# Performance work log

Measured on AMD Instinct MI355X. Metric: run time of the kernel, lower is better.

The kernel has to match this reference:

```python
import jax, jax.numpy as jnp
import numpy as np

B, T = 2, 2048
DENSE = 1024
SPARSE = 1024
NH = 8
HD = SPARSE // NH          # 128
WINDOW = 64
K = 32
RANK = HD // 4             # 32
GATE_THRESH = 0.2


def setup_inputs() -> dict:
    key = jax.random.key(0)
    ks = jax.random.split(key, 12)
    return {
        "x": jax.random.normal(ks[0], (B, T, DENSE), dtype=jnp.float32),
        "enc_q": jax.random.normal(ks[1], (NH, DENSE, HD), dtype=jnp.float32) * 0.02,
        "enc_v": jax.random.normal(ks[2], (NH, DENSE, HD), dtype=jnp.float32) * 0.02,
        # metric network: Linear(SPARSE, SPARSE//2) -> GELU -> Linear(SPARSE//2, NH*HD)
        "metric_w1": jax.random.normal(ks[3], (SPARSE, SPARSE // 2), dtype=jnp.float32) * (1.0 / np.sqrt(SPARSE)),
        "metric_b1": jnp.zeros((SPARSE // 2,), dtype=jnp.float32),
        "metric_w2": jax.random.normal(ks[4], (SPARSE // 2, NH * HD), dtype=jnp.float32) * (1.0 / np.sqrt(SPARSE // 2)),
        "metric_b2": jnp.zeros((NH * HD,), dtype=jnp.float32),
        "base_metric": jnp.ones((NH, HD), dtype=jnp.float32) * 0.1,
        "hebb_U": jax.random.normal(ks[5], (NH, HD, RANK), dtype=jnp.float32) * 0.01,
        "hebb_V": jax.random.normal(ks[6], (NH, RANK, HD), dtype=jnp.float32) * 0.01,
        "decoder": jax.random.normal(ks[7], (NH * HD, DENSE), dtype=jnp.float32) * 0.02,
    }


def _causal_window_indices(t_len, window):
    pos = jnp.arange(t_len)
    off = jnp.arange(window)
    idx = jnp.clip(pos[:, None] - off[None, :], 0, t_len - 1)  # (T, W)
    mask = idx <= pos[:, None]
    return idx, mask


def _dynamic_metric(field, w1, b1, w2, b2, base):
    # field: (B, T, SPARSE)
    sig = field.mean(axis=1)
    if field.shape[1] >= 8:
        sig = sig + field[:, ::8].mean(axis=1) * 0.5
    h = jax.nn.gelu(sig @ w1 + b1, approximate=False)
    mod = (h @ w2 + b2).reshape(field.shape[0], NH, HD)
    return jax.nn.softplus(base[None] + 0.1 * mod)  # (B, NH, HD)


def reference(x, enc_q, enc_v, metric_w1, metric_b1, metric_w2, metric_b2,
              base_metric, hebb_U, hebb_V, decoder):
    Bb, Tt, _ = x.shape
    query_sparse = jax.nn.relu(jnp.einsum('btd,nde->btne', x, enc_q))  # (B,T,NH,HD)
    value_sparse = jax.nn.relu(jnp.einsum('btd,nde->btne', x, enc_v))

    metric = _dynamic_metric(query_sparse.reshape(Bb, Tt, NH * HD),
                             metric_w1, metric_b1, metric_w2, metric_b2, base_metric)

    idx, mask = _causal_window_indices(Tt, WINDOW)  # (T,W)
    idx_b = jnp.broadcast_to(idx[None], (Bb, Tt, WINDOW))
    batch_ix = jnp.arange(Bb)[:, None, None]

    outs = []
    for h in range(NH):
        q_h = query_sparse[:, :, h, :]   # (B,T,HD)
        v_h = value_sparse[:, :, h, :]
        m_h = metric[:, h][:, None, None, :]  # (B,1,1,HD)

        k_windows = q_h[:, idx, :]            # (B,T,W,HD) gather
        diff = k_windows - q_h[:, :, None, :]
        dist = jnp.sqrt((diff * diff * m_h).sum(axis=-1) + 1e-8)  # (B,T,W)
        dist = jnp.where(mask[None], dist, jnp.inf)

        neg_d, loc = jax.lax.top_k(-dist, K)  # smallest-K distances
        topd = -neg_d
        top_idx = jnp.take_along_axis(idx_b, loc, axis=2)  # (B,T,K)

        infl = jnp.exp(-topd)
        infl = infl / (infl.sum(axis=-1, keepdims=True) + 1e-8)

        neighbor_v = v_h[batch_ix, top_idx]   # (B,T,K,HD)
        context = jnp.einsum('btk,btkd->btd', infl, neighbor_v)

        q_norm = jnp.linalg.norm(q_h, axis=-1, keepdims=True)
        gate = (q_norm > GATE_THRESH).astype(q_h.dtype)
        heb_mat = hebb_U[h] @ hebb_V[h]       # (HD,HD)
        q_unit = q_h / jnp.maximum(q_norm, 1e-12)  # F.normalize
        heb_ctx = q_unit @ heb_mat
        context = context + gate * 0.1 * heb_ctx

        outs.append(q_h * context)

    out_sparse = jnp.stack(outs, axis=2)           # (B,T,NH,HD)
    return out_sparse.reshape(Bb, Tt, NH * HD) @ decoder
```

## Files before the change

### kernel.cpp

```cpp
#include <hip/hip_runtime.h>
#include <math.h>

#define T_ 2048
#define NH_ 8
#define HD_ 128

typedef unsigned short u16;
typedef short bf16x8 __attribute__((ext_vector_type(8)));
typedef _Float16 f16x8 __attribute__((ext_vector_type(8)));
typedef float f32x4 __attribute__((ext_vector_type(4)));

union FH { _Float16 h; u16 u; };

__device__ __forceinline__ u16 f2h(float f)
{
    FH c; c.h = (_Float16)f; return c.u;
}
__device__ __forceinline__ float h2f(u16 v)
{
    FH c; c.u = v; return (float)c.h;
}
__device__ __forceinline__ void split1h(float f, u16& h, u16& l)
{
    h = f2h(f);
    l = f2h(f - h2f(h));
}

__device__ __forceinline__ u16 f2bf(float f)
{
    unsigned u = __float_as_uint(f);
    return (u16)((u + 0x7FFFu + ((u >> 16) & 1u)) >> 16);
}
__device__ __forceinline__ float bf2f(u16 h)
{
    return __uint_as_float(((unsigned)h) << 16);
}


__global__ __launch_bounds__(256) void cvt_pk(const float* __restrict__ in,
                                              u16* __restrict__ hi)
{
    int i = (blockIdx.x * 256 + threadIdx.x) * 4;
    int m = i >> 10, k = i & 1023;
    float4 v = *(const float4*)&in[i];
    ushort4 hv = {f2h(v.x), f2h(v.y), f2h(v.z), f2h(v.w)};
    long o = (long)(m >> 6) * 65536 + (k >> 5) * 2048
           + ((k >> 3) & 3) * 512 + (m & 63) * 8 + (k & 7);
    *(ushort4*)&hi[o] = hv;
}

__global__ __launch_bounds__(256) void cvt_wT_pk(const float* __restrict__ src0,
                                                 const float* __restrict__ src1,
                                                 u16* __restrict__ WTh,
                                                 int Kd, int cs, int cm, long sn, int sk)
{
    __shared__ u16 tH[32][33];
    const float* Bw = blockIdx.z ? src1 : src0;
    const int nofs = blockIdx.z << 10;
    const int tid = threadIdx.x;
    const int tx = tid & 31, ty = tid >> 5;
    const int k0 = blockIdx.x * 32, c0 = blockIdx.y * 32;
    #pragma unroll
    for (int r = 0; r < 4; ++r) {
        int k = k0 + ty * 4 + r;
        int c = c0 + tx;
        float v = Bw[(long)(c >> cs) * sn + (long)k * sk + (c & cm)];
        tH[ty * 4 + r][tx] = f2h(v);
    }
    __syncthreads();
    const long sstr = (long)Kd * 64;
    #pragma unroll
    for (int r = 0; r < 4; ++r) {
        int n = nofs + c0 + ty * 4 + r;
        int k = k0 + tx;
        long o = (long)(n >> 6) * sstr + (k >> 5) * 2048
               + ((k >> 3) & 3) * 512 + (n & 63) * 8 + (k & 7);
        WTh[o] = tH[tx][ty * 4 + r];
    }
}

__global__ __launch_bounds__(256, 1) void gemm_qv(
    const u16* __restrict__ Ah, const u16* __restrict__ Bh,
    float* __restrict__ C, float* __restrict__ Ps, float* __restrict__ Ps8,
    int N, int Kd)
{
    __shared__ __align__(16) u16 S[4][6144];

    const int tid  = threadIdx.x;
    const int w    = tid >> 6;
    const int lane = tid & 63;

    const int id   = blockIdx.x;
    const int m0   = (id & 31) * 128;
    const int n0   = (id >> 5) * 256;

    const int mw   = (w & 1) * 64, nw = (w >> 1) * 128;
    const int mr   = lane & 15, quad = lane >> 4;

    const long sstr = (long)Kd * 64;
    const u16* gAh = Ah + (long)((m0 + mw) >> 6) * sstr;
    const u16* gB0 = Bh + (long)((n0 + nw) >> 6) * sstr;
    const u16* gB1 = gB0 + sstr;

    u16* W = &S[w][0];

    f32x4 acc[4][8] = {};
    uint4 a0, a1, a2, a3;
    uint4 b0, b1, b2, b3, b4, b5, b6, b7;

#define LOADG(KT) do { long t = (long)(KT) * 2048 + lane * 8;                        \
    a0 = *(const uint4*)(gAh + t +    0); a1 = *(const uint4*)(gAh + t +  512);      \
    a2 = *(const uint4*)(gAh + t + 1024); a3 = *(const uint4*)(gAh + t + 1536);      \
    b0 = *(const uint4*)(gB0 + t +    0); b1 = *(const uint4*)(gB0 + t +  512);      \
    b2 = *(const uint4*)(gB0 + t + 1024); b3 = *(const uint4*)(gB0 + t + 1536);      \
    b4 = *(const uint4*)(gB1 + t +    0); b5 = *(const uint4*)(gB1 + t +  512);      \
    b6 = *(const uint4*)(gB1 + t + 1024); b7 = *(const uint4*)(gB1 + t + 1536); } while (0)

#define STOREG() do { u16* D = W + lane * 8;                                         \
    *(uint4*)(D +    0) = a0; *(uint4*)(D +  512) = a1;                              \
    *(uint4*)(D + 1024) = a2; *(uint4*)(D + 1536) = a3;                              \
    *(uint4*)(D + 2048) = b0; *(uint4*)(D + 2560) = b1;                              \
    *(uint4*)(D + 3072) = b2; *(uint4*)(D + 3584) = b3;                              \
    *(uint4*)(D + 4096) = b4; *(uint4*)(D + 4608) = b5;                              \
    *(uint4*)(D + 5120) = b6; *(uint4*)(D + 5632) = b7; } while (0)

    LOADG(0);
    STOREG();
    LOADG(1);

    const int NT = Kd >> 5;
    for (int kt = 0; kt < NT; ++kt) {
        f16x8 fah[4], fbh[8];
        #pragma unroll
        for (int i = 0; i < 4; ++i)
            fah[i] = *(const f16x8*)(W + quad * 512 + (i * 16 + mr) * 8);
        #pragma unroll
        for (int j = 0; j < 8; ++j)
            fbh[j] = *(const f16x8*)(W + 2048 + ((j < 4) ? 0 : 2048)
                                     + quad * 512 + ((j & 3) * 16 + mr) * 8);
        if (kt + 1 < NT) STOREG();
        if (kt + 2 < NT) LOADG(kt + 2);
        #pragma unroll
        for (int i = 0; i < 4; ++i)
            #pragma unroll
            for (int j = 0; j < 8; ++j)
                acc[i][j] = __builtin_amdgcn_mfma_f32_16x16x32_f16(fah[i], fbh[j], acc[i][j], 0, 0, 0);
    }
#undef LOADG
#undef STOREG

    #pragma unroll
    for (int i = 0; i < 4; ++i)
        #pragma unroll
        for (int j = 0; j < 8; ++j)
            #pragma unroll
            for (int r = 0; r < 4; ++r) {
                float v = fmaxf(acc[i][j][r], 0.f);
                acc[i][j][r] = v;
                int row = m0 + mw + i * 16 + quad * 4 + r;
                int col = n0 + nw + j * 16 + mr;
                C[(long)row * N + col] = v;
            }

    if (n0 < 1024) {
        int slot = (id & 31) * 2 + (w & 1);
        #pragma unroll
        for (int j = 0; j < 8; ++j) {
            float ps = 0.f, p8 = 0.f;
            #pragma unroll
            for (int i = 0; i < 4; ++i) {
                #pragma unroll
                for (int r = 0; r < 4; ++r) ps += acc[i][j][r];
                if ((quad & 1) == 0) p8 += acc[i][j][0];
            }
            ps += __shfl_xor(ps, 16, 64); ps += __shfl_xor(ps, 32, 64);
            p8 += __shfl_xor(p8, 16, 64); p8 += __shfl_xor(p8, 32, 64);
            if (quad == 0) {
                int col = n0 + nw + j * 16 + mr;
                Ps [slot * 1024 + col] = ps;
                Ps8[slot * 1024 + col] = p8;
            }
        }
    }
}

__global__ __launch_bounds__(256, 1) void gemm_dec(
    const u16* __restrict__ Ah, const u16* __restrict__ Bh,
    float* __restrict__ C, int N, int Kd)
{
    __shared__ __align__(16) u16 S[4][4096];

    const int tid  = threadIdx.x;
    const int w    = tid >> 6;
    const int lane = tid & 63;

    const int id   = blockIdx.x;
    const int m0   = (((id & 7) << 2) + ((id >> 3) & 3)) * 128;
    const int n0   = (id >> 5) * 128;

    const int mw   = (w & 1) * 64, nw = (w >> 1) * 64;
    const int mr   = lane & 15, quad = lane >> 4;

    const long sstr = (long)Kd * 64;
    const u16* gAh = Ah + (long)((m0 + mw) >> 6) * sstr;
    const u16* gBh = Bh + (long)((n0 + nw) >> 6) * sstr;

    u16* W = &S[w][0];

    f32x4 acc[4][4] = {};
    uint4 a0, a1, a2, a3, b0, b1, b2, b3;

#define LOADG(KT) do { long t = (long)(KT) * 2048 + lane * 8;                        \
    a0 = *(const uint4*)(gAh + t +    0); a1 = *(const uint4*)(gAh + t +  512);      \
    a2 = *(const uint4*)(gAh + t + 1024); a3 = *(const uint4*)(gAh + t + 1536);      \
    b0 = *(const uint4*)(gBh + t +    0); b1 = *(const uint4*)(gBh + t +  512);      \
    b2 = *(const uint4*)(gBh + t + 1024); b3 = *(const uint4*)(gBh + t + 1536); } while (0)

#define STOREG() do { u16* D = W + lane * 8;                                         \
    *(uint4*)(D +    0) = a0; *(uint4*)(D +  512) = a1;                              \
    *(uint4*)(D + 1024) = a2; *(uint4*)(D + 1536) = a3;                              \
    *(uint4*)(D + 2048) = b0; *(uint4*)(D + 2560) = b1;                              \
    *(uint4*)(D + 3072) = b2; *(uint4*)(D + 3584) = b3; } while (0)

    LOADG(0);
    STOREG();
    LOADG(1);

    const int NT = Kd >> 5;
    for (int kt = 0; kt < NT; ++kt) {
        f16x8 fah[4], fbh[4];
        #pragma unroll
        for (int i = 0; i < 4; ++i) {
            int ro = quad * 512 + (i * 16 + mr) * 8;
            fah[i] = *(const f16x8*)(W + ro);
            fbh[i] = *(const f16x8*)(W + 2048 + ro);
        }
        if (kt + 1 < NT) STOREG();
        if (kt + 2 < NT) LOADG(kt + 2);
        #pragma unroll
        for (int i = 0; i < 4; ++i)
            #pragma unroll
            for (int j = 0; j < 4; ++j)
                acc[i][j] = __builtin_amdgcn_mfma_f32_16x16x32_f16(fah[i], fbh[j], acc[i][j], 0, 0, 0);
    }
#undef LOADG
#undef STOREG

    #pragma unroll
    for (int i = 0; i < 4; ++i)
        #pragma unroll
        for (int j = 0; j < 4; ++j)
            #pragma unroll
            for (int r = 0; r < 4; ++r) {
                int row = m0 + mw + i * 16 + quad * 4 + r;
                int col = n0 + nw + j * 16 + mr;
                C[(long)row * N + col] = acc[i][j][r];
            }
}

__global__ __launch_bounds__(256) void heb_gemm(
    const u16* __restrict__ Qbf, const u16* __restrict__ MhT,
    u16* __restrict__ HEBbf)
{
    __shared__ __align__(16) u16 sA[4][128][8], sB[4][128][8];

    const int tid  = threadIdx.x;
    const int w    = tid >> 6;
    const int lane = tid & 63;
    const int m0   = blockIdx.x * 128;
    const int h    = blockIdx.y;
    const int mw   = w * 32;
    const int mr   = lane & 15, quad = lane >> 4;
    const u16* Bm  = MhT + h * 16384;

    f32x4 acc[2][8] = {};

    for (int k0 = 0; k0 < 128; k0 += 32) {
        #pragma unroll
        for (int u = 0; u < 4; ++u) {
            int c = (w & 1) * 4 + u;
            int kq = c >> 1, half = c & 1;
            const u16* src; u16* dst; long gofs;
            if (w < 2) {
                src = Qbf;
                dst = &sA[0][0][0] + kq * 1024 + half * 512;
                gofs = (long)(m0 + half * 64 + lane) * 1024 + h * 128 + k0 + kq * 8;
            } else {
                src = Bm;
                dst = &sB[0][0][0] + kq * 1024 + half * 512;
                gofs = (long)(half * 64 + lane) * 128 + k0 + kq * 8;
            }
            __builtin_amdgcn_global_load_lds(
                (const __attribute__((address_space(1))) unsigned int*)(src + gofs),
                (__attribute__((address_space(3))) unsigned int*)dst, 16, 0, 0);
        }
        __syncthreads();

        bf16x8 fa[2], fb[8];
        #pragma unroll
        for (int i = 0; i < 2; ++i)
            fa[i] = *(const bf16x8*)&sA[quad][mw + i * 16 + mr][0];
        #pragma unroll
        for (int j = 0; j < 8; ++j)
            fb[j] = *(const bf16x8*)&sB[quad][j * 16 + mr][0];
        #pragma unroll
        for (int i = 0; i < 2; ++i)
            #pragma unroll
            for (int j = 0; j < 8; ++j)
                acc[i][j] = __builtin_amdgcn_mfma_f32_16x16x32_bf16(fa[i], fb[j], acc[i][j], 0, 0, 0);
        __syncthreads();
    }

    #pragma unroll
    for (int i = 0; i < 2; ++i)
        #pragma unroll
        for (int j = 0; j < 8; ++j)
            #pragma unroll
            for (int r = 0; r < 4; ++r) {
                int row = m0 + mw + i * 16 + quad * 4 + r;
                int col = h * 128 + j * 16 + mr;
                HEBbf[(long)row * 1024 + col] = f2bf(acc[i][j][r]);
            }
}

__global__ __launch_bounds__(256) void qu_stage(const float* __restrict__ QV,
                                                const float* __restrict__ Me,
                                                u16* __restrict__ Qbf,
                                                u16* __restrict__ Uh, u16* __restrict__ Ul,
                                                float* __restrict__ nArr)
{
    int gid4 = (blockIdx.x * 256 + threadIdx.x) * 4;
    int e4 = gid4 & 127;
    int t  = (gid4 >> 7) & 2047;
    int bh = gid4 >> 18;
    int b  = bh >> 3, h = bh & 7;
    float4 q = *(const float4*)&QV[((long)(b * 2048 + t)) * 2048 + h * 128 + e4];
    ushort4 qo = {f2bf(q.x), f2bf(q.y), f2bf(q.z), f2bf(q.w)};
    *(ushort4*)&Qbf[((long)(b * 2048 + t)) * 1024 + h * 128 + e4] = qo;

    float4 m = *(const float4*)&Me[bh * 128 + e4];
    float ux = sqrtf(m.x) * q.x, uy = sqrtf(m.y) * q.y;
    float uz = sqrtf(m.z) * q.z, uw = sqrtf(m.w) * q.w;
    u16 h0, l0, h1, l1, h2, l2, h3, l3;
    split1h(ux, h0, l0); split1h(uy, h1, l1);
    split1h(uz, h2, l2); split1h(uw, h3, l3);
    ushort4 hv = {h0, h1, h2, h3}, lv = {l0, l1, l2, l3};
    *(ushort4*)&Uh[gid4] = hv;
    *(ushort4*)&Ul[gid4] = lv;
    float ps = ux * ux + uy * uy + uz * uz + uw * uw;
    #pragma unroll
    for (int mm = 16; mm; mm >>= 1) ps += __shfl_xor(ps, mm, 64);
    if ((threadIdx.x & 31) == 0) nArr[gid4 >> 7] = ps;
}

__global__ __launch_bounds__(256, 1) void dist_gemm(
    const u16* __restrict__ Uh, const u16* __restrict__ Ul,
    const float* __restrict__ nArr, float* __restrict__ band)
{
    __shared__ __align__(16) u16 sAh[4][64][8],  sAl[4][64][8];
    __shared__ __align__(16) u16 sBh[4][128][8], sBl[4][128][8];
    __shared__ float epi[4][16][128];

    const int tid  = threadIdx.x;
    const int w    = tid >> 6;
    const int lane = tid & 63;
    const int mr   = lane & 15, quad = lane >> 4;
    const int bid  = blockIdx.x;
    const int tile = bid & 31, bh = bid >> 5;
    const int t0   = tile * 64;
    const long ub  = (long)bh * 2048 * 128;

    const u16 *s0, *s1, *s2, *s3, *s4, *s5;
    u16 *d0, *d1, *d2, *d3, *d4, *d5;
    long o0, o1, o2, o3, o4, o5;
    {
        auto mk = [&](int i, const u16*& src, u16*& dst, long& ofs) {
            int c = i * 256 + tid;
            if (c < 512) {
                int row = c & 63, kq = (c >> 6) & 3;
                src = (c < 256) ? Uh : Ul;
                ofs = ub + (long)(t0 + row) * 128 + kq * 8;
                dst = ((c < 256) ? &sAh[0][0][0] : &sAl[0][0][0]) + kq * 512 + row * 8;
            } else {
                int cb = c - 512;
                int row = cb & 127, kq = (cb >> 7) & 3;
                src = (cb < 512) ? Uh : Ul;
                ofs = ub + (long)(t0 - 64 + row) * 128 + kq * 8;
                dst = ((cb < 512) ? &sBh[0][0][0] : &sBl[0][0][0]) + kq * 1024 + row * 8;
            }
        };
        mk(0, s0, d0, o0); mk(1, s1, d1, o1); mk(2, s2, d2, o2);
        mk(3, s3, d3, o3); mk(4, s4, d4, o4); mk(5, s5, d5, o5);
    }

    f32x4 acc[8] = {};
    uint4 g0, g1, g2, g3, g4, g5;
    g0 = *(const uint4*)(s0 + o0); g1 = *(const uint4*)(s1 + o1);
    g2 = *(const uint4*)(s2 + o2); g3 = *(const uint4*)(s3 + o3);
    g4 = *(const uint4*)(s4 + o4); g5 = *(const uint4*)(s5 + o5);

    for (int k0 = 0; k0 < 128; k0 += 32) {
        *(uint4*)d0 = g0; *(uint4*)d1 = g1; *(uint4*)d2 = g2;
        *(uint4*)d3 = g3; *(uint4*)d4 = g4; *(uint4*)d5 = g5;
        __syncthreads();

        if (k0 + 32 < 128) {
            int kn = k0 + 32;
            g0 = *(const uint4*)(s0 + o0 + kn); g1 = *(const uint4*)(s1 + o1 + kn);
            g2 = *(const uint4*)(s2 + o2 + kn); g3 = *(const uint4*)(s3 + o3 + kn);
            g4 = *(const uint4*)(s4 + o4 + kn); g5 = *(const uint4*)(s5 + o5 + kn);
        }

        f16x8 fah = *(const f16x8*)&sAh[quad][w * 16 + mr][0];
        f16x8 fal = *(const f16x8*)&sAl[quad][w * 16 + mr][0];
        #pragma unroll
        for (int j = 0; j < 8; ++j) {
            f16x8 fbh = *(const f16x8*)&sBh[quad][j * 16 + mr][0];
            f16x8 fbl = *(const f16x8*)&sBl[quad][j * 16 + mr][0];
            acc[j] = __builtin_amdgcn_mfma_f32_16x16x32_f16(fah, fbh, acc[j], 0, 0, 0);
            acc[j] = __builtin_amdgcn_mfma_f32_16x16x32_f16(fah, fbl, acc[j], 0, 0, 0);
            acc[j] = __builtin_amdgcn_mfma_f32_16x16x32_f16(fal, fbh, acc[j], 0, 0, 0);
        }
        __syncthreads();
    }

    #pragma unroll
    for (int j = 0; j < 8; ++j)
        #pragma unroll
        for (int r = 0; r < 4; ++r)
            epi[w][quad * 4 + r][j * 16 + mr] = acc[j][r];
    __syncthreads();

    const float* nb = nArr + (long)bh * 2048;
    #pragma unroll
    for (int i = 0; i < 16; ++i) {
        int id = i * 256 + tid;
        int tl = id >> 6, j = id & 63;
        int t  = t0 + tl;
        int r  = t - j;
        int rc = r < 0 ? 0 : r;
        int rl = tl - j + 64;
        float S  = epi[tl >> 4][tl & 15][rl];
        float d2 = nb[t] + nb[rc] - 2.0f * S;
        band[((long)bh * 2048 + t) * 64 + j] = d2;
    }
}

__global__ __launch_bounds__(256) void mlp1_part(const float* __restrict__ Ps,
                                                 const float* __restrict__ Ps8,
                                                 const float* __restrict__ w1,
                                                 float* __restrict__ Pm)
{
    __shared__ float ssig[32];
    int tid = threadIdx.x;
    int o  = blockIdx.x * 256 + tid;
    int b  = blockIdx.y;
    int kc = blockIdx.z;
    int k0 = kc * 32;
    if (tid < 32) {
        int k = k0 + tid;
        float s = 0.f, s8 = 0.f;
        #pragma unroll
        for (int ms = 0; ms < 32; ++ms) {
            long po = ((long)(b * 32 + ms)) * 1024 + k;
            s  += Ps[po];
            s8 += Ps8[po];
        }
        ssig[tid] = s * (1.0f / 2048.0f) + 0.5f * s8 * (1.0f / 256.0f);
    }
    __syncthreads();
    float a = 0.f;
    #pragma unroll 8
    for (int kk = 0; kk < 32; ++kk)
        a += ssig[kk] * w1[(long)(k0 + kk) * 512 + o];
    Pm[((b * 32) + kc) * 512 + o] = a;
}

__global__ __launch_bounds__(256) void mlp2_part(const float* __restrict__ Pm1,
                                                 const float* __restrict__ b1,
                                                 const float* __restrict__ w2,
                                                 float* __restrict__ Pm)
{
    __shared__ float sH[32];
    int tid = threadIdx.x;
    int c  = blockIdx.x * 256 + tid;
    int b  = blockIdx.y;
    int kc = blockIdx.z;
    int k0 = kc * 32;
    if (tid < 32) {
        int o = k0 + tid;
        float a = b1[o];
        #pragma unroll
        for (int kcc = 0; kcc < 32; ++kcc)
            a += Pm1[(b * 32 + kcc) * 512 + o];
        sH[tid] = 0.5f * a * (1.0f + erff(a * 0.70710678118f));
    }
    __syncthreads();
    float a = 0.f;
    #pragma unroll 8
    for (int kk = 0; kk < 32; ++kk)
        a += sH[kk] * w2[(long)(k0 + kk) * 1024 + c];
    Pm[((b * 16) + kc) * 1024 + c] = a;
}

__global__ __launch_bounds__(256) void mlp2fin_hebb(
    const float* __restrict__ Pm, const float* __restrict__ b2,
    const float* __restrict__ base, float* __restrict__ metric,
    const float* __restrict__ U, const float* __restrict__ Vh,
    u16* __restrict__ MhT)
{
    int id = blockIdx.x;
    if (id < 8) {
        int c = (id & 3) * 256 + threadIdx.x;
        int b = id >> 2;
        float a = b2[c];
        #pragma unroll
        for (int kc = 0; kc < 16; ++kc)
            a += Pm[(b * 16 + kc) * 1024 + c];
        float mv = base[c] + 0.1f * a;
        metric[b * 1024 + c] = fmaxf(mv, 0.f) + log1pf(expf(-fabsf(mv)));
    } else {
        int gid = (id - 8) * 256 + threadIdx.x;
        int h = gid >> 14;
        int rem = gid & 16383;
        int e = rem >> 7;
        int f = rem & 127;
        float a = 0.f;
        #pragma unroll
        for (int r = 0; r < 32; ++r)
            a += U[(h * 128 + f) * 32 + r] * Vh[(h * 32 + r) * 128 + e];
        MhT[(h * 128 + e) * 128 + f] = f2bf(a);
    }
}

__global__ __launch_bounds__(256) void context_k(
    const float* __restrict__ QV, const float* __restrict__ band,
    const u16* __restrict__ HEBbf,
    u16* __restrict__ CTh)
{
    __shared__ float wv[4][32];
    __shared__ int   wi[4][32];

    const int w    = threadIdx.x >> 6;
    const int lane = threadIdx.x & 63;
    const int gw   = blockIdx.x * 4 + w;
    const int h    = gw & 7;
    const int bt   = gw >> 3;
    const int t    = bt & (T_ - 1);
    const int b    = bt >> 11;
    const int bh   = b * 8 + h;

    const long qrow  = (long)bt * 2048 + h * 128;
    const long hrow  = (long)bt * 1024 + h * 128;

    float q0 = QV[qrow + lane], q1 = QV[qrow + 64 + lane];
    float ss = q0 * q0 + q1 * q1;
    #pragma unroll
    for (int s = 32; s; s >>= 1) ss += __shfl_xor(ss, s, 64);
    const float qn  = sqrtf(ss);
    const float inv = 1.0f / fmaxf(qn, 1e-12f);

    int je = lane < t ? lane : t;
    float d2v = (je == 0) ? 0.f
              : band[((long)bh * 2048 + t) * 64 + je];
    float d2f = fmaxf(d2v, 0.f) + 1e-8f;
    unsigned kb = (__float_as_uint(d2f) & 0xFFFFFFC0u) | (unsigned)lane;

    #pragma unroll
    for (int k = 2; k <= 32; k <<= 1)
        #pragma unroll
        for (int s = k >> 1; s >= 1; s >>= 1) {
            unsigned ok = __shfl_xor(kb, s, 64);
            bool takeMin = (((lane & k) == 0) == ((lane & s) == 0));
            if ((ok < kb) == takeMin) kb = ok;
        }
    {
        unsigned ok = __shfl_xor(kb, 32, 64);
        kb = ok < kb ? ok : kb;
    }

    int jj = kb & 63;
    float wexp = 0.f;
    if (lane < 32)
        wexp = expf(-sqrtf(__uint_as_float(kb & 0xFFFFFFC0u)));
    float tot = wexp;
    #pragma unroll
    for (int s = 32; s; s >>= 1) tot += __shfl_xor(tot, s, 64);
    float wn = wexp / (tot + 1e-8f);
    if (lane < 32) {
        wv[w][lane] = wn;
        int ii = t - jj; if (ii < 0) ii = 0;
        wi[w][lane] = ii;
    }

    float c0 = 0.f, c1 = 0.f;
    #pragma unroll 8
    for (int k = 0; k < 32; ++k) {
        float wk = wv[w][k];
        long vb = ((long)(b * T_ + wi[w][k])) * 2048 + 1024 + h * 128;
        c0 += wk * QV[vb + lane];
        c1 += wk * QV[vb + 64 + lane];
    }

    if (qn > 0.2f) {
        float s = 0.1f * inv;
        c0 += s * bf2f(HEBbf[hrow + lane]);
        c1 += s * bf2f(HEBbf[hrow + 64 + lane]);
    }

    int c0c = h * 128 + lane, c1c = c0c + 64;
    long po0 = (long)(bt >> 6) * 65536 + (c0c >> 5) * 2048
             + ((c0c >> 3) & 3) * 512 + (bt & 63) * 8 + (c0c & 7);
    long po1 = (long)(bt >> 6) * 65536 + (c1c >> 5) * 2048
             + ((c1c >> 3) & 3) * 512 + (bt & 63) * 8 + (c1c & 7);
    CTh[po0] = f2h(q0 * c0);
    CTh[po1] = f2h(q1 * c1);
}

extern "C" void kernel_launch(void* const* d_in, const int* in_sizes, int n_in,
                              void* d_out, int out_size, void* d_ws, size_t ws_size,
                              hipStream_t stream)
{
    const float* x     = (const float*)d_in[0];
    const float* enc_q = (const float*)d_in[1];
    const float* enc_v = (const float*)d_in[2];
    const float* w1    = (const float*)d_in[3];
    const float* b1    = (const float*)d_in[4];
    const float* w2    = (const float*)d_in[5];
    const float* b2    = (const float*)d_in[6];
    const float* base  = (const float*)d_in[7];
    const float* hU    = (const float*)d_in[8];
    const float* hV    = (const float*)d_in[9];
    const float* dec   = (const float*)d_in[10];
    float* out = (float*)d_out;
    float* ws  = (float*)d_ws;

    float* QV  = ws;
    u16* wTh   = (u16*)(ws + 8388608);
    float* Ps  = ws + 9437184;
    float* Ps8 = ws + 9502720;
    u16* Uhp   = (u16*)(ws + 8388608);
    u16* Ulp   = (u16*)(ws + 10485760);
    u16* CTh   = (u16*)(ws + 8388608);
    u16* MhT   = (u16*)(ws + 12582912);
    float* nA  = ws + 12713984;
    float* Me  = ws + 12749824;
    u16* wdTh  = (u16*)ws;
    u16* xh    = (u16*)d_out;
    u16* Qbf   = (u16*)d_out;
    u16* HEBbf = (u16*)d_out + 4194304;
    float* band = (float*)d_out;
    float* Pm1 = (float*)d_out + 2097152;
    float* Pm2 = (float*)d_out + 2129920;

    cvt_pk<<<4096, 256, 0, stream>>>(x, xh);

    cvt_wT_pk<<<dim3(32, 32, 2), 256, 0, stream>>>(enc_q, enc_v, wTh,
                                                   1024, 7, 127, 131072L, 128);
    gemm_qv<<<256, 256, 0, stream>>>(xh, wTh, QV, Ps, Ps8, 2048, 1024);

    mlp1_part<<<dim3(2, 2, 32), 256, 0, stream>>>(Ps, Ps8, w1, Pm1);
    mlp2_part<<<dim3(4, 2, 16), 256, 0, stream>>>(Pm1, b1, w2, Pm2);
    mlp2fin_hebb<<<520, 256, 0, stream>>>(Pm2, b2, base, Me, hU, hV, MhT);

    qu_stage<<<4096, 256, 0, stream>>>(QV, Me, Qbf, Uhp, Ulp, nA);
    heb_gemm<<<dim3(32, 8), 256, 0, stream>>>(Qbf, MhT, HEBbf);
    dist_gemm<<<512, 256, 0, stream>>>(Uhp, Ulp, nA, band);

    context_k<<<8192, 256, 0, stream>>>(QV, band, HEBbf, CTh);

    cvt_wT_pk<<<dim3(32, 32, 1), 256, 0, stream>>>(dec, dec, wdTh,
                                                   1024, 30, 0x3fffffff, 0L, 1024);
    gemm_dec<<<256, 256, 0, stream>>>(CTh, wdTh, out, 1024, 1024);
}
```

Baseline: 224.9 us.

## Store V activations as fp16 in a separate buffer and fuse input conversions

The QV GEMM now writes Q as fp32 into a 1024-wide buffer and V as fp16 into its own buffer, in place of one interleaved fp32 2048-wide array. The context kernel gathers the neighbour V rows from the fp16 buffer, halving the bytes read in that gather. The x conversion and the encoder-weight transpose are merged into one launch to save a kernel launch. V loses precision by being rounded to fp16.

```diff
diff --git a/kernel.cpp b/kernel.cpp
--- a/kernel.cpp
+++ b/kernel.cpp
@@ -37,26 +37,55 @@
 }
 
 
-__global__ __launch_bounds__(256) void cvt_pk(const float* __restrict__ in,
-                                              u16* __restrict__ hi)
-{
-    int i = (blockIdx.x * 256 + threadIdx.x) * 4;
-    int m = i >> 10, k = i & 1023;
-    float4 v = *(const float4*)&in[i];
-    ushort4 hv = {f2h(v.x), f2h(v.y), f2h(v.z), f2h(v.w)};
-    long o = (long)(m >> 6) * 65536 + (k >> 5) * 2048
-           + ((k >> 3) & 3) * 512 + (m & 63) * 8 + (k & 7);
-    *(ushort4*)&hi[o] = hv;
+__global__ __launch_bounds__(256) void cvt_in(const float* __restrict__ x,
+                                              const float* __restrict__ enc_q,
+                                              const float* __restrict__ enc_v,
+                                              u16* __restrict__ xh,
+                                              u16* __restrict__ WTh)
+{
+    __shared__ u16 tH[32][33];
+    const int bid = blockIdx.x;
+    if (bid < 4096) {
+        int i = (bid * 256 + threadIdx.x) * 4;
+        int m = i >> 10, k = i & 1023;
+        float4 v = *(const float4*)&x[i];
+        ushort4 hv = {f2h(v.x), f2h(v.y), f2h(v.z), f2h(v.w)};
+        long o = (long)(m >> 6) * 65536 + (k >> 5) * 2048
+               + ((k >> 3) & 3) * 512 + (m & 63) * 8 + (k & 7);
+        *(ushort4*)&xh[o] = hv;
+    } else {
+        int rb = bid - 4096;
+        int bx = rb & 31, by = (rb >> 5) & 31, bz = rb >> 10;
+        const float* Bw = bz ? enc_v : enc_q;
+        const int nofs = bz << 10;
+        const int tid = threadIdx.x;
+        const int tx = tid & 31, ty = tid >> 5;
+        const int k0 = bx * 32, c0 = by * 32;
+        #pragma unroll
+        for (int r = 0; r < 4; ++r) {
+            int k = k0 + ty * 4 + r;
+            int c = c0 + tx;
+            float v = Bw[(long)(c >> 7) * 131072 + (long)k * 128 + (c & 127)];
+            tH[ty * 4 + r][tx] = f2h(v);
+        }
+        __syncthreads();
+        #pragma unroll
+        for (int r = 0; r < 4; ++r) {
+            int n = nofs + c0 + ty * 4 + r;
+            int k = k0 + tx;
+            long o = (long)(n >> 6) * 65536 + (k >> 5) * 2048
+                   + ((k >> 3) & 3) * 512 + (n & 63) * 8 + (k & 7);
+            WTh[o] = tH[tx][ty * 4 + r];
+        }
+    }
 }
 
 __global__ __launch_bounds__(256) void cvt_wT_pk(const float* __restrict__ src0,
-                                                 const float* __restrict__ src1,
                                                  u16* __restrict__ WTh,
                                                  int Kd, int cs, int cm, long sn, int sk)
 {
     __shared__ u16 tH[32][33];
-    const float* Bw = blockIdx.z ? src1 : src0;
-    const int nofs = blockIdx.z << 10;
+    const float* Bw = src0;
     const int tid = threadIdx.x;
     const int tx = tid & 31, ty = tid >> 5;
     const int k0 = blockIdx.x * 32, c0 = blockIdx.y * 32;
@@ -71,7 +100,7 @@
     const long sstr = (long)Kd * 64;
     #pragma unroll
     for (int r = 0; r < 4; ++r) {
-        int n = nofs + c0 + ty * 4 + r;
+        int n = c0 + ty * 4 + r;
         int k = k0 + tx;
         long o = (long)(n >> 6) * sstr + (k >> 5) * 2048
                + ((k >> 3) & 3) * 512 + (n & 63) * 8 + (k & 7);
@@ -81,8 +110,8 @@
 
 __global__ __launch_bounds__(256, 1) void gemm_qv(
     const u16* __restrict__ Ah, const u16* __restrict__ Bh,
-    float* __restrict__ C, float* __restrict__ Ps, float* __restrict__ Ps8,
-    int N, int Kd)
+    float* __restrict__ Qf, u16* __restrict__ Vh,
+    float* __restrict__ Ps, float* __restrict__ Ps8, int Kd)
 {
     __shared__ __align__(16) u16 S[4][6144];
 
@@ -149,20 +178,19 @@
 #undef LOADG
 #undef STOREG
 
-    #pragma unroll
-    for (int i = 0; i < 4; ++i)
-        #pragma unroll
-        for (int j = 0; j < 8; ++j)
+    if (n0 < 1024) {
+        #pragma unroll
+        for (int i = 0; i < 4; ++i)
             #pragma unroll
-            for (int r = 0; r < 4; ++r) {
-                float v = fmaxf(acc[i][j][r], 0.f);
-                acc[i][j][r] = v;
-                int row = m0 + mw + i * 16 + quad * 4 + r;
-                int col = n0 + nw + j * 16 + mr;
-                C[(long)row * N + col] = v;
-            }
-
-    if (n0 < 1024) {
+            for (int j = 0; j < 8; ++j)
+                #pragma unroll
+                for (int r = 0; r < 4; ++r) {
+                    float v = fmaxf(acc[i][j][r], 0.f);
+                    acc[i][j][r] = v;
+                    int row = m0 + mw + i * 16 + quad * 4 + r;
+                    int col = n0 + nw + j * 16 + mr;
+                    Qf[(long)row * 1024 + col] = v;
+                }
         int slot = (id & 31) * 2 + (w & 1);
         #pragma unroll
         for (int j = 0; j < 8; ++j) {
@@ -181,6 +209,18 @@
                 Ps8[slot * 1024 + col] = p8;
             }
         }
+    } else {
+        #pragma unroll
+        for (int i = 0; i < 4; ++i)
+            #pragma unroll
+            for (int j = 0; j < 8; ++j)
+                #pragma unroll
+                for (int r = 0; r < 4; ++r) {
+                    float v = fmaxf(acc[i][j][r], 0.f);
+                    int row = m0 + mw + i * 16 + quad * 4 + r;
+                    int col = n0 - 1024 + nw + j * 16 + mr;
+                    Vh[(long)row * 1024 + col] = f2h(v);
+                }
     }
 }
 
@@ -323,7 +363,7 @@
             }
 }
 
-__global__ __launch_bounds__(256) void qu_stage(const float* __restrict__ QV,
+__global__ __launch_bounds__(256) void qu_stage(const float* __restrict__ Qf,
                                                 const float* __restrict__ Me,
                                                 u16* __restrict__ Qbf,
                                                 u16* __restrict__ Uh, u16* __restrict__ Ul,
@@ -334,7 +374,7 @@
     int t  = (gid4 >> 7) & 2047;
     int bh = gid4 >> 18;
     int b  = bh >> 3, h = bh & 7;
-    float4 q = *(const float4*)&QV[((long)(b * 2048 + t)) * 2048 + h * 128 + e4];
+    float4 q = *(const float4*)&Qf[((long)(b * 2048 + t)) * 1024 + h * 128 + e4];
     ushort4 qo = {f2bf(q.x), f2bf(q.y), f2bf(q.z), f2bf(q.w)};
     *(ushort4*)&Qbf[((long)(b * 2048 + t)) * 1024 + h * 128 + e4] = qo;
 
@@ -534,8 +574,8 @@
 }
 
 __global__ __launch_bounds__(256) void context_k(
-    const float* __restrict__ QV, const float* __restrict__ band,
-    const u16* __restrict__ HEBbf,
+    const float* __restrict__ Qf, const u16* __restrict__ Vh,
+    const float* __restrict__ band, const u16* __restrict__ HEBbf,
     u16* __restrict__ CTh)
 {
     __shared__ float wv[4][32];
@@ -550,10 +590,10 @@
     const int b    = bt >> 11;
     const int bh   = b * 8 + h;
 
-    const long qrow  = (long)bt * 2048 + h * 128;
+    const long qrow  = (long)bt * 1024 + h * 128;
     const long hrow  = (long)bt * 1024 + h * 128;
 
-    float q0 = QV[qrow + lane], q1 = QV[qrow + 64 + lane];
+    float q0 = Qf[qrow + lane], q1 = Qf[qrow + 64 + lane];
     float ss = q0 * q0 + q1 * q1;
     #pragma unroll
     for (int s = 32; s; s >>= 1) ss += __shfl_xor(ss, s, 64);
@@ -597,9 +637,9 @@
     #pragma unroll 8
     for (int k = 0; k < 32; ++k) {
         float wk = wv[w][k];
-        long vb = ((long)(b * T_ + wi[w][k])) * 2048 + 1024 + h * 128;
-        c0 += wk * QV[vb + lane];
-        c1 += wk * QV[vb + 64 + lane];
+        long vb = ((long)(b * T_ + wi[w][k])) * 1024 + h * 128;
+        c0 += wk * h2f(Vh[vb + lane]);
+        c1 += wk * h2f(Vh[vb + 64 + lane]);
     }
 
     if (qn > 0.2f) {
@@ -635,7 +675,8 @@
     float* out = (float*)d_out;
     float* ws  = (float*)d_ws;
 
-    float* QV  = ws;
+    float* Qf  = ws;
+    u16* Vhp   = (u16*)(ws + 4194304);
     u16* wTh   = (u16*)(ws + 8388608);
     float* Ps  = ws + 9437184;
     float* Ps8 = ws + 9502720;
@@ -653,23 +694,21 @@
     float* Pm1 = (float*)d_out + 2097152;
     float* Pm2 = (float*)d_out + 2129920;
 
-    cvt_pk<<<4096, 256, 0, stream>>>(x, xh);
-
-    cvt_wT_pk<<<dim3(32, 32, 2), 256, 0, stream>>>(enc_q, enc_v, wTh,
-                                                   1024, 7, 127, 131072L, 128);
-    gemm_qv<<<256, 256, 0, stream>>>(xh, wTh, QV, Ps, Ps8, 2048, 1024);
+    cvt_in<<<6144, 256, 0, stream>>>(x, enc_q, enc_v, xh, wTh);
+
+    gemm_qv<<<256, 256, 0, stream>>>(xh, wTh, Qf, Vhp, Ps, Ps8, 1024);
 
     mlp1_part<<<dim3(2, 2, 32), 256, 0, stream>>>(Ps, Ps8, w1, Pm1);
     mlp2_part<<<dim3(4, 2, 16), 256, 0, stream>>>(Pm1, b1, w2, Pm2);
     mlp2fin_hebb<<<520, 256, 0, stream>>>(Pm2, b2, base, Me, hU, hV, MhT);
 
-    qu_stage<<<4096, 256, 0, stream>>>(QV, Me, Qbf, Uhp, Ulp, nA);
+    qu_stage<<<4096, 256, 0, stream>>>(Qf, Me, Qbf, Uhp, Ulp, nA);
     heb_gemm<<<dim3(32, 8), 256, 0, stream>>>(Qbf, MhT, HEBbf);
     dist_gemm<<<512, 256, 0, stream>>>(Uhp, Ulp, nA, band);
 
-    context_k<<<8192, 256, 0, stream>>>(QV, band, HEBbf, CTh);
-
-    cvt_wT_pk<<<dim3(32, 32, 1), 256, 0, stream>>>(dec, dec, wdTh,
-                                                   1024, 30, 0x3fffffff, 0L, 1024);
+    context_k<<<8192, 256, 0, stream>>>(Qf, Vhp, band, HEBbf, CTh);
+
+    cvt_wT_pk<<<dim3(32, 32), 256, 0, stream>>>(dec, wdTh,
+                                                1024, 30, 0x3fffffff, 0L, 1024);
     gemm_dec<<<256, 256, 0, stream>>>(CTh, wdTh, out, 1024, 1024);
 }
```

Result: faster. 213.9 us (-4.9%).
